# Performance work log

Measured on AMD Instinct MI355X. Metric: run time of the kernel, lower is better.

The kernel has to match this reference:

```python
import jax, jax.numpy as jnp
import numpy as np

H = 128          # hidden_size
L = 3            # num_layers
N = 200_000      # total atoms across all fragments
E = 400_000      # bidirectional bonds (avg degree ~2)
G = 8192         # number of molecular subgraphs
ATOM_V = 120
BOND_V = 5


def setup_inputs() -> dict:
    key = jax.random.key(0)
    ks = jax.random.split(key, 14)
    s = 1.0 / np.sqrt(H)
    f = lambda k, shp: (jax.random.normal(k, shp, jnp.float32) * s)
    return {
        "atom_types": jax.random.randint(ks[0], (N,), 0, ATOM_V),
        "edges": jax.random.randint(ks[1], (2, E), 0, N),
        "edge_types": jax.random.randint(ks[2], (E,), 0, BOND_V),
        "node_batch": jnp.sort(jax.random.randint(ks[3], (N,), 0, G)),
        "atom_emb": f(ks[4], (ATOM_V, H)),
        "bond_emb": f(ks[5], (BOND_V, H)),
        "conv_w1": f(ks[6], (L, H, H)),
        "conv_b1": jnp.zeros((L, H), jnp.float32),
        "conv_w2": f(ks[7], (L, H, H)),
        "conv_b2": jnp.zeros((L, H), jnp.float32),
        "proj_w1": f(ks[8], (H, H)),
        "proj_b1": jnp.zeros((H,), jnp.float32),
        "proj_w2": f(ks[9], (H, H)),
        "proj_b2": jnp.zeros((H,), jnp.float32),
    }


def reference(atom_types, edges, edge_types, node_batch,
              atom_emb, bond_emb,
              conv_w1, conv_b1, conv_w2, conv_b2,
              proj_w1, proj_b1, proj_w2, proj_b2):
    # node / bond embeddings (torch clamps indices to vocab-1)
    x = atom_emb[jnp.clip(atom_types, 0, ATOM_V - 1)]       # [N, H]
    a = bond_emb[jnp.clip(edge_types, 0, BOND_V - 1)]       # [E, H]
    src, dst = edges[0], edges[1]
    # GINEConv layers: x_i' = MLP(x_i + sum_{j->i} ReLU(x_j + e_ji)), eps=0
    for l in range(L):
        m = jax.nn.relu(x[src] + a)                         # [E, H] edge messages
        agg = jax.ops.segment_sum(m, dst, num_segments=N)   # scatter-add to dst nodes
        h = x + agg
        h = jax.nn.relu(h @ conv_w1[l] + conv_b1[l])
        x = h @ conv_w2[l] + conv_b2[l]
    # per-graph mean readout
    sums = jax.ops.segment_sum(x, node_batch, num_segments=G)                      # [G, H]
    cnt = jax.ops.segment_sum(jnp.ones((N, 1), x.dtype), node_batch, num_segments=G)
    g = sums / jnp.maximum(cnt, 1.0)
    # proj: Linear -> SiLU -> Linear
    g = jax.nn.silu(g @ proj_w1 + proj_b1)
    return g @ proj_w2 + proj_b2                            # [G, H]
```

## Files before the change

### kernel.cpp

```cpp
#include <hip/hip_runtime.h>

typedef unsigned short u16;
typedef __attribute__((ext_vector_type(8))) short short8;
typedef __attribute__((ext_vector_type(4))) float f32x4;

#define HDIM 128
#define SCAN_B 512

__device__ __forceinline__ float bf2f(u16 v) {
    return __uint_as_float(((unsigned int)v) << 16);
}
__device__ __forceinline__ u16 f2bf(float f) {
    unsigned int u = __float_as_uint(f);
    unsigned int r = (u + 0x7FFFu + ((u >> 16) & 1u)) >> 16;
    return (u16)r;
}

__global__ __launch_bounds__(256) void prep_kernel(
    const float* __restrict__ w1, const float* __restrict__ w2,
    const float* __restrict__ pw1, const float* __restrict__ pw2,
    const float* __restrict__ atom_emb,
    u16* __restrict__ wt, u16* __restrict__ ebf)
{
    int gid = blockIdx.x * 256 + threadIdx.x;
    if (gid < 8 * 16384) {
        int mat = gid >> 14;
        int idx = gid & 16383;
        int n = idx >> 7, k = idx & 127;
        const float* src;
        if      (mat < 3) src = w1 + mat * 16384;
        else if (mat < 6) src = w2 + (mat - 3) * 16384;
        else if (mat == 6) src = pw1;
        else               src = pw2;
        wt[gid] = f2bf(src[k * 128 + n]);
    } else {
        int i = gid - 8 * 16384;
        if (i < 120 * 128) ebf[i] = f2bf(atom_emb[i]);
    }
}

__global__ __launch_bounds__(256) void deg_hist_kernel(
    const int* __restrict__ edges, int* __restrict__ deg, int E, int N)
{
    int e = blockIdx.x * 256 + threadIdx.x;
    if (e >= E) return;
    int d = edges[E + e];
    d = d < 0 ? 0 : (d >= N ? N - 1 : d);
    atomicAdd(&deg[d], 1);
}

__global__ __launch_bounds__(SCAN_B) void scan_block_kernel(
    const int* __restrict__ deg, int* __restrict__ offs, int* __restrict__ bsum, int N)
{
    __shared__ int tmp[SCAN_B];
    int t = threadIdx.x;
    int gid = blockIdx.x * SCAN_B + t;
    int v = (gid < N) ? deg[gid] : 0;
    tmp[t] = v;
    __syncthreads();
#pragma unroll
    for (int off = 1; off < SCAN_B; off <<= 1) {
        int add = (t >= off) ? tmp[t - off] : 0;
        __syncthreads();
        tmp[t] += add;
        __syncthreads();
    }
    if (gid < N) offs[gid] = tmp[t] - v;
    if (t == SCAN_B - 1) bsum[blockIdx.x] = tmp[t];
}

__global__ __launch_bounds__(256) void finalize_offs_kernel(
    int* __restrict__ offs, const int* __restrict__ bsum,
    int* __restrict__ cursor, int N, int E)
{
    __shared__ int red[256];
    const int tid = threadIdx.x;
    const int B = blockIdx.x >> 1;
    int sum = 0;
    for (int t = tid; t < B; t += 256) sum += bsum[t];
    red[tid] = sum;
    __syncthreads();
#pragma unroll
    for (int off = 128; off > 0; off >>= 1) {
        if (tid < off) red[tid] += red[tid + off];
        __syncthreads();
    }
    int prefix = red[0];
    int gid = blockIdx.x * 256 + tid;
    if (gid < N) {
        int v = offs[gid] + prefix;
        offs[gid] = v;
        cursor[gid] = v;
    }
    if (gid == 0) offs[N] = E;
}

__global__ __launch_bounds__(256) void fill_csr_kernel(
    const int* __restrict__ edges, const int* __restrict__ etypes,
    int* __restrict__ cursor, int* __restrict__ csr, int E, int N)
{
    int e = blockIdx.x * 256 + threadIdx.x;
    if (e >= E) return;
    int s = edges[e], d = edges[E + e], t = etypes[e];
    s = s < 0 ? 0 : (s >= N ? N - 1 : s);
    d = d < 0 ? 0 : (d >= N ? N - 1 : d);
    t = t < 0 ? 0 : (t > 4 ? 4 : t);
    int pos = atomicAdd(&cursor[d], 1);
    csr[pos] = (s << 3) | t;
}

__global__ __launch_bounds__(512, 4) void gine_kernel(
    const u16* __restrict__ x_in, u16* __restrict__ x_out,
    const int* __restrict__ types, int use_emb, const u16* __restrict__ ebf,
    const int* __restrict__ offs, const int* __restrict__ csr,
    const float* __restrict__ bond_emb,
    const u16* __restrict__ w1t, const float* __restrict__ b1,
    const u16* __restrict__ w2t, const float* __restrict__ b2, int N)
{
    __shared__ __align__(16) u16 As[128][136];
    __shared__ __align__(16) u16 Ws[128][136];
    __shared__ __align__(16) u16 bsh[5 * 128];
    const int tid  = threadIdx.x;
    const int row0 = blockIdx.x * 128;
    const int wave = tid >> 6, lane = tid & 63;
    const int m = lane & 15, quad = lane >> 4;

    for (int i = tid; i < 640; i += 512) bsh[i] = f2bf(bond_emb[i]);
    {
        const uint4* src = (const uint4*)w1t;
        for (int i = tid; i < 2048; i += 512) {
            int n = i >> 4, k8 = i & 15;
            *(uint4*)&Ws[n][k8 * 8] = src[i];
        }
    }
    {
        const int rp = tid >> 4, c8 = (tid & 15) * 8;
        __syncthreads();

        int rowA = row0 + rp,      rowB = row0 + 32 + rp;
        int rowC = row0 + 64 + rp, rowD = row0 + 96 + rp;
        int rcA = rowA < N ? rowA : N - 1;
        int rcB = rowB < N ? rowB : N - 1;
        int rcC = rowC < N ? rowC : N - 1;
        int rcD = rowD < N ? rowD : N - 1;
        const u16 *spA, *spB, *spC, *spD;
        if (use_emb) {
            int tA = types[rcA]; tA = tA < 0 ? 0 : (tA > 119 ? 119 : tA);
            int tB = types[rcB]; tB = tB < 0 ? 0 : (tB > 119 ? 119 : tB);
            int tC = types[rcC]; tC = tC < 0 ? 0 : (tC > 119 ? 119 : tC);
            int tD = types[rcD]; tD = tD < 0 ? 0 : (tD > 119 ? 119 : tD);
            spA = ebf + (size_t)tA * 128; spB = ebf + (size_t)tB * 128;
            spC = ebf + (size_t)tC * 128; spD = ebf + (size_t)tD * 128;
        } else {
            spA = x_in + (size_t)rcA * 128; spB = x_in + (size_t)rcB * 128;
            spC = x_in + (size_t)rcC * 128; spD = x_in + (size_t)rcD * 128;
        }
        int jbA = offs[rcA], jeA = rowA < N ? offs[rcA + 1] : jbA;
        int jbB = offs[rcB], jeB = rowB < N ? offs[rcB + 1] : jbB;
        int jbC = offs[rcC], jeC = rowC < N ? offs[rcC + 1] : jbC;
        int jbD = offs[rcD], jeD = rowD < N ? offs[rcD + 1] : jbD;
        uint4 svA = *(const uint4*)(spA + c8);
        uint4 svB = *(const uint4*)(spB + c8);
        uint4 svC = *(const uint4*)(spC + c8);
        uint4 svD = *(const uint4*)(spD + c8);
        float accA[8], accB[8], accC[8], accD[8];
        {
            const u16* pA = (const u16*)&svA; const u16* pB = (const u16*)&svB;
            const u16* pC = (const u16*)&svC; const u16* pD = (const u16*)&svD;
#pragma unroll
            for (int i = 0; i < 8; i++) {
                accA[i] = bf2f(pA[i]); accB[i] = bf2f(pB[i]);
                accC[i] = bf2f(pC[i]); accD[i] = bf2f(pD[i]);
            }
        }
        int dA = jeA - jbA, dB = jeB - jbB, dC = jeC - jbC, dD = jeD - jbD;
        int dmax = dA > dB ? dA : dB;
        dmax = dC > dmax ? dC : dmax;
        dmax = dD > dmax ? dD : dmax;
        for (int k = 0; k < dmax; k += 2) {
            bool a0 = k < dA,     a1 = (k + 1) < dA;
            bool a2 = k < dB,     a3 = (k + 1) < dB;
            bool a4 = k < dC,     a5 = (k + 1) < dC;
            bool a6 = k < dD,     a7 = (k + 1) < dD;
            int v0 = a0 ? csr[jbA + k] : 0;  int v1 = a1 ? csr[jbA + k + 1] : 0;
            int v2 = a2 ? csr[jbB + k] : 0;  int v3 = a3 ? csr[jbB + k + 1] : 0;
            int v4 = a4 ? csr[jbC + k] : 0;  int v5 = a5 ? csr[jbC + k + 1] : 0;
            int v6 = a6 ? csr[jbD + k] : 0;  int v7 = a7 ? csr[jbD + k + 1] : 0;
            const u16 *p0, *p1, *p2, *p3, *p4, *p5, *p6, *p7;
            if (use_emb) {
                int t0 = types[v0 >> 3]; t0 = t0 < 0 ? 0 : (t0 > 119 ? 119 : t0);
                int t1 = types[v1 >> 3]; t1 = t1 < 0 ? 0 : (t1 > 119 ? 119 : t1);
                int t2 = types[v2 >> 3]; t2 = t2 < 0 ? 0 : (t2 > 119 ? 119 : t2);
                int t3 = types[v3 >> 3]; t3 = t3 < 0 ? 0 : (t3 > 119 ? 119 : t3);
                int t4 = types[v4 >> 3]; t4 = t4 < 0 ? 0 : (t4 > 119 ? 119 : t4);
                int t5 = types[v5 >> 3]; t5 = t5 < 0 ? 0 : (t5 > 119 ? 119 : t5);
                int t6 = types[v6 >> 3]; t6 = t6 < 0 ? 0 : (t6 > 119 ? 119 : t6);
                int t7 = types[v7 >> 3]; t7 = t7 < 0 ? 0 : (t7 > 119 ? 119 : t7);
                p0 = ebf + (size_t)t0 * 128; p1 = ebf + (size_t)t1 * 128;
                p2 = ebf + (size_t)t2 * 128; p3 = ebf + (size_t)t3 * 128;
                p4 = ebf + (size_t)t4 * 128; p5 = ebf + (size_t)t5 * 128;
                p6 = ebf + (size_t)t6 * 128; p7 = ebf + (size_t)t7 * 128;
            } else {
                p0 = x_in + (size_t)(v0 >> 3) * 128; p1 = x_in + (size_t)(v1 >> 3) * 128;
                p2 = x_in + (size_t)(v2 >> 3) * 128; p3 = x_in + (size_t)(v3 >> 3) * 128;
                p4 = x_in + (size_t)(v4 >> 3) * 128; p5 = x_in + (size_t)(v5 >> 3) * 128;
                p6 = x_in + (size_t)(v6 >> 3) * 128; p7 = x_in + (size_t)(v7 >> 3) * 128;
            }
            uint4 g0 = *(const uint4*)(p0 + c8);
            uint4 g1 = *(const uint4*)(p1 + c8);
            uint4 g2 = *(const uint4*)(p2 + c8);
            uint4 g3 = *(const uint4*)(p3 + c8);
            uint4 g4 = *(const uint4*)(p4 + c8);
            uint4 g5 = *(const uint4*)(p5 + c8);
            uint4 g6 = *(const uint4*)(p6 + c8);
            uint4 g7 = *(const uint4*)(p7 + c8);
            if (a0) { const u16* gp = (const u16*)&g0; const u16* bp = bsh + (v0 & 7) * 128 + c8;
#pragma unroll
                for (int i = 0; i < 8; i++) { float mm = bf2f(gp[i]) + bf2f(bp[i]); accA[i] += mm > 0.f ? mm : 0.f; } }
            if (a1) { const u16* gp = (const u16*)&g1; const u16* bp = bsh + (v1 & 7) * 128 + c8;
#pragma unroll
                for (int i = 0; i < 8; i++) { float mm = bf2f(gp[i]) + bf2f(bp[i]); accA[i] += mm > 0.f ? mm : 0.f; } }
            if (a2) { const u16* gp = (const u16*)&g2; const u16* bp = bsh + (v2 & 7) * 128 + c8;
#pragma unroll
                for (int i = 0; i < 8; i++) { float mm = bf2f(gp[i]) + bf2f(bp[i]); accB[i] += mm > 0.f ? mm : 0.f; } }
            if (a3) { const u16* gp = (const u16*)&g3; const u16* bp = bsh + (v3 & 7) * 128 + c8;
#pragma unroll
                for (int i = 0; i < 8; i++) { float mm = bf2f(gp[i]) + bf2f(bp[i]); accB[i] += mm > 0.f ? mm : 0.f; } }
            if (a4) { const u16* gp = (const u16*)&g4; const u16* bp = bsh + (v4 & 7) * 128 + c8;
#pragma unroll
                for (int i = 0; i < 8; i++) { float mm = bf2f(gp[i]) + bf2f(bp[i]); accC[i] += mm > 0.f ? mm : 0.f; } }
            if (a5) { const u16* gp = (const u16*)&g5; const u16* bp = bsh + (v5 & 7) * 128 + c8;
#pragma unroll
                for (int i = 0; i < 8; i++) { float mm = bf2f(gp[i]) + bf2f(bp[i]); accC[i] += mm > 0.f ? mm : 0.f; } }
            if (a6) { const u16* gp = (const u16*)&g6; const u16* bp = bsh + (v6 & 7) * 128 + c8;
#pragma unroll
                for (int i = 0; i < 8; i++) { float mm = bf2f(gp[i]) + bf2f(bp[i]); accD[i] += mm > 0.f ? mm : 0.f; } }
            if (a7) { const u16* gp = (const u16*)&g7; const u16* bp = bsh + (v7 & 7) * 128 + c8;
#pragma unroll
                for (int i = 0; i < 8; i++) { float mm = bf2f(gp[i]) + bf2f(bp[i]); accD[i] += mm > 0.f ? mm : 0.f; } }
        }
        uint4 ovA = make_uint4(0u,0u,0u,0u), ovB = ovA, ovC = ovA, ovD = ovA;
        if (rowA < N) { u16* op = (u16*)&ovA;
#pragma unroll
            for (int i = 0; i < 8; i++) op[i] = f2bf(accA[i]); }
        if (rowB < N) { u16* op = (u16*)&ovB;
#pragma unroll
            for (int i = 0; i < 8; i++) op[i] = f2bf(accB[i]); }
        if (rowC < N) { u16* op = (u16*)&ovC;
#pragma unroll
            for (int i = 0; i < 8; i++) op[i] = f2bf(accC[i]); }
        if (rowD < N) { u16* op = (u16*)&ovD;
#pragma unroll
            for (int i = 0; i < 8; i++) op[i] = f2bf(accD[i]); }
        *(uint4*)&As[rp][c8]      = ovA;
        *(uint4*)&As[32 + rp][c8] = ovB;
        *(uint4*)&As[64 + rp][c8] = ovC;
        *(uint4*)&As[96 + rp][c8] = ovD;
    }
    __syncthreads();

    f32x4 acc[8];
#pragma unroll
    for (int c = 0; c < 8; c++) acc[c] = (f32x4){0.f, 0.f, 0.f, 0.f};
#pragma unroll
    for (int q = 0; q < 4; q++) {
        short8 a = *(const short8*)&As[wave * 16 + m][q * 32 + quad * 8];
#pragma unroll
        for (int c = 0; c < 8; c++) {
            short8 b = *(const short8*)&Ws[c * 16 + m][q * 32 + quad * 8];
            acc[c] = __builtin_amdgcn_mfma_f32_16x16x32_bf16(a, b, acc[c], 0, 0, 0);
        }
    }
    __syncthreads();
    {
        const uint4* src = (const uint4*)w2t;
        for (int i = tid; i < 2048; i += 512) {
            int n = i >> 4, k8 = i & 15;
            *(uint4*)&Ws[n][k8 * 8] = src[i];
        }
    }
#pragma unroll
    for (int c = 0; c < 8; c++) {
        int col = c * 16 + m;
        float bias = b1[col];
#pragma unroll
        for (int r = 0; r < 4; r++) {
            float v = acc[c][r] + bias;
            v = v > 0.f ? v : 0.f;
            As[wave * 16 + quad * 4 + r][col] = f2bf(v);
        }
    }
    __syncthreads();
    f32x4 acc2[8];
#pragma unroll
    for (int c = 0; c < 8; c++) acc2[c] = (f32x4){0.f, 0.f, 0.f, 0.f};
#pragma unroll
    for (int q = 0; q < 4; q++) {
        short8 a = *(const short8*)&As[wave * 16 + m][q * 32 + quad * 8];
#pragma unroll
        for (int c = 0; c < 8; c++) {
            short8 b = *(const short8*)&Ws[c * 16 + m][q * 32 + quad * 8];
            acc2[c] = __builtin_amdgcn_mfma_f32_16x16x32_bf16(a, b, acc2[c], 0, 0, 0);
        }
    }
    __syncthreads();
#pragma unroll
    for (int c = 0; c < 8; c++) {
        int col = c * 16 + m;
        float bias = b2[col];
#pragma unroll
        for (int r = 0; r < 4; r++)
            As[wave * 16 + quad * 4 + r][col] = f2bf(acc2[c][r] + bias);
    }
    __syncthreads();
    for (int i = tid; i < 2048; i += 512) {
        int r = i >> 4, c8 = (i & 15) * 8;
        int row = row0 + r;
        if (row < N) *(uint4*)(x_out + (size_t)row * 128 + c8) = *(const uint4*)&As[r][c8];
    }
}

__global__ __launch_bounds__(256) void readout_proj_kernel(
    const u16* __restrict__ x, const int* __restrict__ nb,
    const u16* __restrict__ pw1t, const float* __restrict__ pb1,
    const u16* __restrict__ pw2t, const float* __restrict__ pb2,
    float* __restrict__ out, int N, int G)
{
    __shared__ __align__(16) u16 As[64][136];
    __shared__ __align__(16) u16 Ws[128][136];
    __shared__ float part[16][128];
    __shared__ int bounds[65];
    const int tid  = threadIdx.x;
    const int g0   = blockIdx.x * 64;
    const int wave = tid >> 6, lane = tid & 63;
    const int m = lane & 15, quad = lane >> 4;

    {
        const uint4* src = (const uint4*)pw1t;
        for (int i = tid; i < 2048; i += 256) {
            int n = i >> 4, k8 = i & 15;
            *(uint4*)&Ws[n][k8 * 8] = src[i];
        }
    }
    if (tid < 65) {
        int target = g0 + tid;
        int lo = 0, hi = N;
        while (lo < hi) {
            int mid = (lo + hi) >> 1;
            if (nb[mid] < target) lo = mid + 1; else hi = mid;
        }
        bounds[tid] = lo;
    }
    __syncthreads();

    const int rp = tid >> 4, c8 = (tid & 15) * 8;
    for (int i = 0; i < 64; i++) {
        int s = bounds[i], e = bounds[i + 1];
        float acc[8];
#pragma unroll
        for (int j = 0; j < 8; j++) acc[j] = 0.f;
        for (int n = s + rp; n < e; n += 16) {
            uint4 v = *(const uint4*)(x + (size_t)n * 128 + c8);
            const u16* vp = (const u16*)&v;
#pragma unroll
            for (int j = 0; j < 8; j++) acc[j] += bf2f(vp[j]);
        }
#pragma unroll
        for (int j = 0; j < 8; j++) part[rp][c8 + j] = acc[j];
        __syncthreads();
        if (tid < 128) {
            float sum = 0.f;
#pragma unroll
            for (int g = 0; g < 16; g++) sum += part[g][tid];
            float cnt = (float)((e - s) > 0 ? (e - s) : 1);
            As[i][tid] = f2bf(sum / cnt);
        }
        __syncthreads();
    }

    f32x4 acc[8];
#pragma unroll
    for (int c = 0; c < 8; c++) acc[c] = (f32x4){0.f, 0.f, 0.f, 0.f};
#pragma unroll
    for (int q = 0; q < 4; q++) {
        short8 a = *(const short8*)&As[wave * 16 + m][q * 32 + quad * 8];
#pragma unroll
        for (int c = 0; c < 8; c++) {
            short8 b = *(const short8*)&Ws[c * 16 + m][q * 32 + quad * 8];
            acc[c] = __builtin_amdgcn_mfma_f32_16x16x32_bf16(a, b, acc[c], 0, 0, 0);
        }
    }
    __syncthreads();
    {
        const uint4* src = (const uint4*)pw2t;
        for (int i = tid; i < 2048; i += 256) {
            int n = i >> 4, k8 = i & 15;
            *(uint4*)&Ws[n][k8 * 8] = src[i];
        }
    }
#pragma unroll
    for (int c = 0; c < 8; c++) {
        int col = c * 16 + m;
        float bias = pb1[col];
#pragma unroll
        for (int r = 0; r < 4; r++) {
            float v = acc[c][r] + bias;
            v = v / (1.f + __expf(-v));
            As[wave * 16 + quad * 4 + r][col] = f2bf(v);
        }
    }
    __syncthreads();
    f32x4 acc2[8];
#pragma unroll
    for (int c = 0; c < 8; c++) acc2[c] = (f32x4){0.f, 0.f, 0.f, 0.f};
#pragma unroll
    for (int q = 0; q < 4; q++) {
        short8 a = *(const short8*)&As[wave * 16 + m][q * 32 + quad * 8];
#pragma unroll
        for (int c = 0; c < 8; c++) {
            short8 b = *(const short8*)&Ws[c * 16 + m][q * 32 + quad * 8];
            acc2[c] = __builtin_amdgcn_mfma_f32_16x16x32_bf16(a, b, acc2[c], 0, 0, 0);
        }
    }
#pragma unroll
    for (int c = 0; c < 8; c++) {
        int col = c * 16 + m;
        float bias = pb2[col];
#pragma unroll
        for (int r = 0; r < 4; r++) {
            int row = g0 + wave * 16 + quad * 4 + r;
            if (row < G) out[(size_t)row * 128 + col] = acc2[c][r] + bias;
        }
    }
}

extern "C" void kernel_launch(void* const* d_in, const int* in_sizes, int n_in,
                              void* d_out, int out_size, void* d_ws, size_t ws_size,
                              hipStream_t stream) {
    const int*   atom_types  = (const int*)d_in[0];
    const int*   edges       = (const int*)d_in[1];
    const int*   edge_types  = (const int*)d_in[2];
    const int*   node_batch  = (const int*)d_in[3];
    const float* atom_emb    = (const float*)d_in[4];
    const float* bond_emb    = (const float*)d_in[5];
    const float* conv_w1     = (const float*)d_in[6];
    const float* conv_b1     = (const float*)d_in[7];
    const float* conv_w2     = (const float*)d_in[8];
    const float* conv_b2     = (const float*)d_in[9];
    const float* pw1         = (const float*)d_in[10];
    const float* pb1         = (const float*)d_in[11];
    const float* pw2         = (const float*)d_in[12];
    const float* pb2         = (const float*)d_in[13];
    float* out = (float*)d_out;

    const int N = in_sizes[0];
    const int E = in_sizes[2];
    const int G = out_size / HDIM;
    const int nblk = (N + SCAN_B - 1) / SCAN_B;

    size_t xA_bytes  = (size_t)N * HDIM * sizeof(u16);
    size_t xB_bytes  = (size_t)N * HDIM * sizeof(u16);
    size_t wt_bytes  = (size_t)8 * HDIM * HDIM * sizeof(u16);
    size_t ebf_bytes = (size_t)120 * HDIM * sizeof(u16);
    size_t deg_bytes = (size_t)N * 4;
    size_t off_bytes = (size_t)(N + 1) * 4;
    size_t cur_bytes = (size_t)N * 4;
    size_t bs_bytes  = (size_t)nblk * 4;
    size_t csr_bytes = (size_t)E * 4;
    size_t need = xA_bytes + xB_bytes + wt_bytes + ebf_bytes +
                  deg_bytes + off_bytes + cur_bytes + bs_bytes + csr_bytes;
    if (ws_size < need) {
        hipMemsetAsync(d_out, 0, (size_t)out_size * sizeof(float), stream);
        return;
    }
    char* p = (char*)d_ws;
    u16* xA   = (u16*)p;  p += xA_bytes;
    u16* xB   = (u16*)p;  p += xB_bytes;
    u16* wt   = (u16*)p;  p += wt_bytes;
    u16* ebf  = (u16*)p;  p += ebf_bytes;
    int* deg  = (int*)p;  p += deg_bytes;
    int* offs = (int*)p;  p += off_bytes;
    int* cur  = (int*)p;  p += cur_bytes;
    int* bsum = (int*)p;  p += bs_bytes;
    int* csr  = (int*)p;

    prep_kernel<<<(8 * 16384 + 120 * 128 + 255) / 256, 256, 0, stream>>>(
        conv_w1, conv_w2, pw1, pw2, atom_emb, wt, ebf);

    hipMemsetAsync(deg, 0, deg_bytes, stream);
    deg_hist_kernel<<<(E + 255) / 256, 256, 0, stream>>>(edges, deg, E, N);
    scan_block_kernel<<<nblk, SCAN_B, 0, stream>>>(deg, offs, bsum, N);
    finalize_offs_kernel<<<(N + 255) / 256, 256, 0, stream>>>(offs, bsum, cur, N, E);
    fill_csr_kernel<<<(E + 255) / 256, 256, 0, stream>>>(edges, edge_types, cur, csr, E, N);

    const int gblocks = (N + 127) / 128;
    gine_kernel<<<gblocks, 512, 0, stream>>>(
        xB , xA, atom_types, 1, ebf, offs, csr, bond_emb,
        wt + 0 * 16384, conv_b1 + 0, wt + 3 * 16384, conv_b2 + 0, N);
    gine_kernel<<<gblocks, 512, 0, stream>>>(
        xA, xB, atom_types, 0, ebf, offs, csr, bond_emb,
        wt + 1 * 16384, conv_b1 + 128, wt + 4 * 16384, conv_b2 + 128, N);
    gine_kernel<<<gblocks, 512, 0, stream>>>(
        xB, xA, atom_types, 0, ebf, offs, csr, bond_emb,
        wt + 2 * 16384, conv_b1 + 256, wt + 5 * 16384, conv_b2 + 256, N);

    readout_proj_kernel<<<(G + 63) / 64, 256, 0, stream>>>(
        xA, node_batch, wt + 6 * 16384, pb1, wt + 7 * 16384, pb2, out, N, G);
}
```

Measured before the change: 394.9 us.

## Split readout into per-graph mean kernel and separate projection kernel

The fused readout+projection kernel previously processed 64 graphs serially per block (128 blocks total), with two barriers per graph. The readout is now a separate kernel with one block per graph (8192 blocks), which writes bf16 means to a workspace buffer. A second kernel loads those means and runs the two MFMA projection layers. The aim is far more parallelism for the memory-bound mean reduction, at the cost of an extra launch and a small intermediate buffer round trip.

Result: faster. 360.0 us (-8.8%).

```diff
diff --git a/kernel.cpp b/kernel.cpp
--- a/kernel.cpp
+++ b/kernel.cpp
@@ -320,18 +320,56 @@
     }
 }
 
-__global__ __launch_bounds__(256) void readout_proj_kernel(
+__global__ __launch_bounds__(256) void readout_mean_kernel(
     const u16* __restrict__ x, const int* __restrict__ nb,
+    u16* __restrict__ gm, int N)
+{
+    __shared__ int range[2];
+    __shared__ float part[16][128];
+    int b = blockIdx.x;
+    int tid = threadIdx.x;
+    if (tid < 2) {
+        int target = b + tid;
+        int lo = 0, hi = N;
+        while (lo < hi) {
+            int mid = (lo + hi) >> 1;
+            if (nb[mid] < target) lo = mid + 1; else hi = mid;
+        }
+        range[tid] = lo;
+    }
+    __syncthreads();
+    int s = range[0], e = range[1];
+    int rg = tid >> 4, c8 = (tid & 15) * 8;
+    float acc[8];
+#pragma unroll
+    for (int i = 0; i < 8; i++) acc[i] = 0.f;
+    for (int n = s + rg; n < e; n += 16) {
+        uint4 v = *(const uint4*)(x + (size_t)n * 128 + c8);
+        const u16* vp = (const u16*)&v;
+#pragma unroll
+        for (int i = 0; i < 8; i++) acc[i] += bf2f(vp[i]);
+    }
+#pragma unroll
+    for (int i = 0; i < 8; i++) part[rg][c8 + i] = acc[i];
+    __syncthreads();
+    if (tid < 128) {
+        float sum = 0.f;
+#pragma unroll
+        for (int g = 0; g < 16; g++) sum += part[g][tid];
+        float cnt = (float)((e - s) > 0 ? (e - s) : 1);
+        gm[(size_t)b * 128 + tid] = f2bf(sum / cnt);
+    }
+}
+
+__global__ __launch_bounds__(256) void proj_kernel(
+    const u16* __restrict__ gm, float* __restrict__ out,
     const u16* __restrict__ pw1t, const float* __restrict__ pb1,
-    const u16* __restrict__ pw2t, const float* __restrict__ pb2,
-    float* __restrict__ out, int N, int G)
+    const u16* __restrict__ pw2t, const float* __restrict__ pb2, int G)
 {
     __shared__ __align__(16) u16 As[64][136];
     __shared__ __align__(16) u16 Ws[128][136];
-    __shared__ float part[16][128];
-    __shared__ int bounds[65];
     const int tid  = threadIdx.x;
-    const int g0   = blockIdx.x * 64;
+    const int row0 = blockIdx.x * 64;
     const int wave = tid >> 6, lane = tid & 63;
     const int m = lane & 15, quad = lane >> 4;
 
@@ -342,42 +380,14 @@
             *(uint4*)&Ws[n][k8 * 8] = src[i];
         }
     }
-    if (tid < 65) {
-        int target = g0 + tid;
-        int lo = 0, hi = N;
-        while (lo < hi) {
-            int mid = (lo + hi) >> 1;
-            if (nb[mid] < target) lo = mid + 1; else hi = mid;
-        }
-        bounds[tid] = lo;
-    }
-    __syncthreads();
-
-    const int rp = tid >> 4, c8 = (tid & 15) * 8;
-    for (int i = 0; i < 64; i++) {
-        int s = bounds[i], e = bounds[i + 1];
-        float acc[8];
-#pragma unroll
-        for (int j = 0; j < 8; j++) acc[j] = 0.f;
-        for (int n = s + rp; n < e; n += 16) {
-            uint4 v = *(const uint4*)(x + (size_t)n * 128 + c8);
-            const u16* vp = (const u16*)&v;
-#pragma unroll
-            for (int j = 0; j < 8; j++) acc[j] += bf2f(vp[j]);
-        }
-#pragma unroll
-        for (int j = 0; j < 8; j++) part[rp][c8 + j] = acc[j];
-        __syncthreads();
-        if (tid < 128) {
-            float sum = 0.f;
-#pragma unroll
-            for (int g = 0; g < 16; g++) sum += part[g][tid];
-            float cnt = (float)((e - s) > 0 ? (e - s) : 1);
-            As[i][tid] = f2bf(sum / cnt);
-        }
-        __syncthreads();
-    }
-
+    for (int i = tid; i < 1024; i += 256) {
+        int r = i >> 4, c8 = (i & 15) * 8;
+        int row = row0 + r;
+        uint4 ov = make_uint4(0u, 0u, 0u, 0u);
+        if (row < G) ov = *(const uint4*)(gm + (size_t)row * 128 + c8);
+        *(uint4*)&As[r][c8] = ov;
+    }
+    __syncthreads();
     f32x4 acc[8];
 #pragma unroll
     for (int c = 0; c < 8; c++) acc[c] = (f32x4){0.f, 0.f, 0.f, 0.f};
@@ -428,7 +438,7 @@
         float bias = pb2[col];
 #pragma unroll
         for (int r = 0; r < 4; r++) {
-            int row = g0 + wave * 16 + quad * 4 + r;
+            int row = row0 + wave * 16 + quad * 4 + r;
             if (row < G) out[(size_t)row * 128 + col] = acc2[c][r] + bias;
         }
     }
@@ -462,12 +472,13 @@
     size_t xB_bytes  = (size_t)N * HDIM * sizeof(u16);
     size_t wt_bytes  = (size_t)8 * HDIM * HDIM * sizeof(u16);
     size_t ebf_bytes = (size_t)120 * HDIM * sizeof(u16);
+    size_t gm_bytes  = (size_t)G * HDIM * sizeof(u16);
     size_t deg_bytes = (size_t)N * 4;
     size_t off_bytes = (size_t)(N + 1) * 4;
     size_t cur_bytes = (size_t)N * 4;
     size_t bs_bytes  = (size_t)nblk * 4;
     size_t csr_bytes = (size_t)E * 4;
-    size_t need = xA_bytes + xB_bytes + wt_bytes + ebf_bytes +
+    size_t need = xA_bytes + xB_bytes + wt_bytes + ebf_bytes + gm_bytes +
                   deg_bytes + off_bytes + cur_bytes + bs_bytes + csr_bytes;
     if (ws_size < need) {
         hipMemsetAsync(d_out, 0, (size_t)out_size * sizeof(float), stream);
@@ -478,6 +489,7 @@
     u16* xB   = (u16*)p;  p += xB_bytes;
     u16* wt   = (u16*)p;  p += wt_bytes;
     u16* ebf  = (u16*)p;  p += ebf_bytes;
+    u16* gm   = (u16*)p;  p += gm_bytes;
     int* deg  = (int*)p;  p += deg_bytes;
     int* offs = (int*)p;  p += off_bytes;
     int* cur  = (int*)p;  p += cur_bytes;
@@ -504,6 +516,7 @@
         xB, xA, atom_types, 0, ebf, offs, csr, bond_emb,
         wt + 2 * 16384, conv_b1 + 256, wt + 5 * 16384, conv_b2 + 256, N);
 
-    readout_proj_kernel<<<(G + 63) / 64, 256, 0, stream>>>(
-        xA, node_batch, wt + 6 * 16384, pb1, wt + 7 * 16384, pb2, out, N, G);
-}
+    readout_mean_kernel<<<G, 256, 0, stream>>>(xA, node_batch, gm, N);
+    proj_kernel<<<(G + 63) / 64, 256, 0, stream>>>(
+        gm, out, wt + 6 * 16384, pb1, wt + 7 * 16384, pb2, G);
+}
```
